# Kernel tuning notes

Hardware: AMD Instinct MI355X
Metric: run time of the kernel (lower is better)

The kernel has to match this reference:

```python
import jax, jax.numpy as jnp
import numpy as np

B, N, DIM, H, DH = 8, 1024, 1024, 16, 64

def setup_inputs() -> dict:
    key = jax.random.key(0)
    ks = jax.random.split(key, 6)
    return {
        'x': jax.random.normal(ks[0], (B, N, DIM), dtype=jnp.float32),
        'freqs': jax.random.normal(ks[1], (1, N, DH), dtype=jnp.float32),
        'bias': jax.random.normal(ks[2], (1, N, DH), dtype=jnp.float32),
        'ln_gamma': jnp.ones((DIM,), jnp.float32),
        'ln_beta': jnp.zeros((DIM,), jnp.float32),
        'w_qk': jax.random.normal(ks[3], (DIM, 2 * H * DH), dtype=jnp.float32) * (DIM ** -0.5),
        'w_v': jax.random.normal(ks[4], (DIM, H * DH), dtype=jnp.float32) * (DIM ** -0.5),
        'w_out': jax.random.normal(ks[5], (H * DH, DIM), dtype=jnp.float32) * ((H * DH) ** -0.5),
        'b_out': jnp.zeros((DIM,), jnp.float32),
    }

def _apply_polar(t, freqs):
    # t: [b,h,n,d]; freqs: [1,n,d] broadcast over b,h. Output doubles last dim.
    t = jax.nn.softplus(t)
    return jnp.concatenate((t * jnp.cos(freqs), t * jnp.sin(freqs)), axis=-1)

def reference(x, freqs, bias, ln_gamma, ln_beta, w_qk, w_v, w_out, b_out):
    eps = 1e-5
    mu = jnp.mean(x, axis=-1, keepdims=True)
    var = jnp.var(x, axis=-1, keepdims=True)
    xn = (x - mu) * jax.lax.rsqrt(var + eps) * ln_gamma + ln_beta
    qk = jnp.einsum('bnd,de->bne', xn, w_qk)
    q, k = jnp.split(qk, 2, axis=-1)
    v = jnp.einsum('bnd,de->bne', xn, w_v)
    split_heads = lambda t: t.reshape(B, N, H, DH).transpose(0, 2, 1, 3)
    q, k, v = split_heads(q), split_heads(k), split_heads(v)
    q = _apply_polar(q, freqs)          # [b,h,n,2*DH]
    k = _apply_polar(k, freqs + bias)   # [b,h,n,2*DH]
    scale = DH ** -0.5
    dots = jnp.einsum('bhnd,bhmd->bhnm', q, k) * scale
    attn = jax.nn.softmax(dots, axis=-1)
    out = jnp.einsum('bhnm,bhmd->bhnd', attn, v)
    out = out.transpose(0, 2, 1, 3).reshape(B, N, H * DH)
    return jnp.einsum('bne,ed->bnd', out, w_out) + b_out
```

## Files before the change

### kernel.cpp

```cpp
#include <hip/hip_runtime.h>
#include <cmath>

using f16   = _Float16;
using f16x2 = __attribute__((ext_vector_type(2))) _Float16;
using f16x4 = __attribute__((ext_vector_type(4))) _Float16;
using f16x8 = __attribute__((ext_vector_type(8))) _Float16;
using f32x4 = __attribute__((ext_vector_type(4))) float;

#define DEV __device__ __forceinline__

constexpr int Bb  = 8;
constexpr int Nn  = 1024;
constexpr int DIM = 1024;
constexpr int Hh  = 16;
constexpr int DH  = 64;
constexpr int EQKV = 3072;

DEV void async16(const f16* g, f16* l) {
  __builtin_amdgcn_global_load_lds(
      (const __attribute__((address_space(1))) void*)g,
      (__attribute__((address_space(3))) void*)l, 16, 0, 0);
}

DEV float softplusf(float x) {
  return fmaxf(x, 0.f) + __logf(1.f + __expf(-fabsf(x)));
}

__global__ __launch_bounds__(256) void transpose_cvt(const float* __restrict__ src,
                                                     f16* __restrict__ dst,
                                                     int rows, int cols) {
  __shared__ float tile[32][33];
  int t = threadIdx.x, tx = t & 31, ty = t >> 5;
  int c0 = blockIdx.x * 32, r0 = blockIdx.y * 32;
#pragma unroll
  for (int j = 0; j < 32; j += 8)
    tile[ty + j][tx] = src[(size_t)(r0 + ty + j) * cols + c0 + tx];
  __syncthreads();
#pragma unroll
  for (int j = 0; j < 32; j += 8)
    dst[(size_t)(c0 + ty + j) * rows + r0 + tx] = (f16)tile[tx][ty + j];
}

__global__ __launch_bounds__(256) void ln_kernel(const float* __restrict__ x,
                                                 const float* __restrict__ gamma,
                                                 const float* __restrict__ beta,
                                                 f16* __restrict__ xn) {
  int row = blockIdx.x;
  int t = threadIdx.x;
  const float4* xr = (const float4*)(x + (size_t)row * DIM);
  float4 v = xr[t];
  float s  = v.x + v.y + v.z + v.w;
  float s2 = v.x * v.x + v.y * v.y + v.z * v.z + v.w * v.w;
#pragma unroll
  for (int off = 32; off; off >>= 1) {
    s  += __shfl_xor(s,  off, 64);
    s2 += __shfl_xor(s2, off, 64);
  }
  __shared__ float red[8];
  int wv = t >> 6, lane = t & 63;
  if (lane == 0) { red[wv] = s; red[4 + wv] = s2; }
  __syncthreads();
  s  = red[0] + red[1] + red[2] + red[3];
  s2 = red[4] + red[5] + red[6] + red[7];
  float mu  = s * (1.f / DIM);
  float var = s2 * (1.f / DIM) - mu * mu;
  float rs  = rsqrtf(var + 1e-5f);
  float4 g = ((const float4*)gamma)[t];
  float4 bb = ((const float4*)beta)[t];
  f16x4 o;
  o[0] = (f16)((v.x - mu) * rs * g.x + bb.x);
  o[1] = (f16)((v.y - mu) * rs * g.y + bb.y);
  o[2] = (f16)((v.z - mu) * rs * g.z + bb.z);
  o[3] = (f16)((v.w - mu) * rs * g.w + bb.w);
  ((f16x4*)(xn + (size_t)row * DIM))[t] = o;
}

template <bool FP32OUT>
__global__ __launch_bounds__(256) void gemm_bt(const f16* __restrict__ A,
                                               const f16* __restrict__ Bt,
                                               void* __restrict__ Cv,
                                               const float* __restrict__ bias,
                                               int M, int K, int E) {
  __shared__ f16 lA[128 * 32];
  __shared__ f16 lB[128 * 32];
  int tid  = threadIdx.x;
  int lane = tid & 63;
  int wv   = __builtin_amdgcn_readfirstlane(tid >> 6);
  int nbe  = E >> 7;
  int bm = blockIdx.x / nbe, be = blockIdx.x % nbe;
  size_t m0 = (size_t)bm * 128, e0 = (size_t)be * 128;
  int wm = (wv & 1) * 64, we = (wv >> 1) * 64;
  int lm = lane & 15, q = lane >> 4;

  f32x4 acc[4][4] = {};

  int row_s[2], cg_s[2];
#pragma unroll
  for (int r = 0; r < 2; ++r) {
    int s = r * 256 + tid;
    row_s[r] = s >> 2;
    cg_s[r]  = (s & 3) ^ ((row_s[r] >> 1) & 3);
  }
  const f16* pa[4];
  const f16* pb[4];
#pragma unroll
  for (int i = 0; i < 4; ++i) {
    int ra = wm + i * 16 + lm;
    pa[i] = lA + ra * 32 + (q ^ ((ra >> 1) & 3)) * 8;
    int rb = we + i * 16 + lm;
    pb[i] = lB + rb * 32 + (q ^ ((rb >> 1) & 3)) * 8;
  }

  for (int k0 = 0; k0 < K; k0 += 32) {
#pragma unroll
    for (int r = 0; r < 2; ++r) {
      const f16* ga = A  + (m0 + row_s[r]) * K + k0 + cg_s[r] * 8;
      const f16* gb = Bt + (e0 + row_s[r]) * K + k0 + cg_s[r] * 8;
      async16(ga, lA + (r * 256 + wv * 64) * 8);
      async16(gb, lB + (r * 256 + wv * 64) * 8);
    }
    __syncthreads();
    f16x8 af[4], bf[4];
#pragma unroll
    for (int i = 0; i < 4; ++i) {
      af[i] = *(const f16x8*)pa[i];
      bf[i] = *(const f16x8*)pb[i];
    }
#pragma unroll
    for (int i = 0; i < 4; ++i)
#pragma unroll
      for (int j = 0; j < 4; ++j)
        acc[i][j] = __builtin_amdgcn_mfma_f32_16x16x32_f16(af[i], bf[j], acc[i][j], 0, 0, 0);
    __syncthreads();
  }

#pragma unroll
  for (int i = 0; i < 4; ++i) {
    size_t mbase = m0 + wm + i * 16 + q * 4;
#pragma unroll
    for (int j = 0; j < 4; ++j) {
      size_t e = e0 + we + j * 16 + lm;
#pragma unroll
      for (int g = 0; g < 4; ++g) {
        float val = acc[i][j][g];
        if (FP32OUT)
          ((float*)Cv)[(mbase + g) * (size_t)E + e] = val + bias[e];
        else
          ((f16*)Cv)[(mbase + g) * (size_t)E + e] = (f16)val;
      }
    }
  }
}

__global__ __launch_bounds__(256) void polar_kernel(const f16* __restrict__ qkv,
                                                    const float* __restrict__ freqs,
                                                    const float* __restrict__ fbias,
                                                    f16* __restrict__ Qp,
                                                    f16* __restrict__ Kp,
                                                    f16* __restrict__ Vt) {
  __shared__ f16 vt[64 * 66];
  int tid = threadIdx.x;
  int bx = blockIdx.x;
  int nt = bx & 15, bh = bx >> 4;
  int b = bh >> 4, h = bh & 15;
  size_t tok0 = (size_t)b * Nn + nt * 64;
  int n0 = nt * 64;
  constexpr float kScale = 0.125f;
#pragma unroll
  for (int i = 0; i < 8; ++i) {
    int e2 = tid + i * 256;
    int nl = e2 >> 5, dp = (e2 & 31) * 2;
    size_t src = (tok0 + nl) * EQKV + h * 64 + dp;
    f16x2 q2 = *(const f16x2*)(qkv + src);
    f16x2 k2 = *(const f16x2*)(qkv + src + 1024);
    f16x2 v2 = *(const f16x2*)(qkv + src + 2048);
    int fidx = (n0 + nl) * 64 + dp;
    float2 f2  = *(const float2*)(freqs + fidx);
    float2 fb2 = *(const float2*)(fbias + fidx);
    f16x2 qc, qs, kc, ksn;
#pragma unroll
    for (int u = 0; u < 2; ++u) {
      float fq = u ? f2.y : f2.x;
      float fk = fq + (u ? fb2.y : fb2.x);
      float spq = softplusf((float)q2[u]) * kScale;
      float spk = softplusf((float)k2[u]);
      float snq, csq, snk, csk;
      __sincosf(fq, &snq, &csq);
      __sincosf(fk, &snk, &csk);
      qc[u]  = (f16)(spq * csq);
      qs[u]  = (f16)(spq * snq);
      kc[u]  = (f16)(spk * csk);
      ksn[u] = (f16)(spk * snk);
    }
    size_t dst = ((size_t)bh * Nn + n0 + nl) * 128 + dp;
    *(f16x2*)(Qp + dst)      = qc;
    *(f16x2*)(Qp + dst + 64) = qs;
    *(f16x2*)(Kp + dst)      = kc;
    *(f16x2*)(Kp + dst + 64) = ksn;
    vt[dp * 66 + nl]       = v2[0];
    vt[(dp + 1) * 66 + nl] = v2[1];
  }
  __syncthreads();
#pragma unroll
  for (int i = 0; i < 16; ++i) {
    int e = tid + i * 256;
    int d = e >> 6, nl = e & 63;
    Vt[((size_t)bh * 64 + d) * Nn + n0 + nl] = vt[d * 66 + nl];
  }
}

constexpr int AK0 = 0;
constexpr int AK1 = 8192;
constexpr int AV0 = 16384;
constexpr int AV1 = 20480;

__global__ __launch_bounds__(512, 6) void attn_kernel(const f16* __restrict__ Qp,
                                                      const f16* __restrict__ Kp,
                                                      const f16* __restrict__ Vt,
                                                      f16* __restrict__ attout) {
  __shared__ f16 smem[24576];

  int tid = threadIdx.x, lane = tid & 63;
  int wv = __builtin_amdgcn_readfirstlane(tid >> 6);
  int lm = lane & 15, q = lane >> 4;
  int bx = blockIdx.x;
  int bh = (bx & 7) | ((bx >> 6) << 3);
  int qt = (bx >> 3) & 7;
  const f16* Kbase = Kp + (size_t)bh * Nn * 128;
  const f16* Vbase = Vt + (size_t)bh * 64 * Nn;

#pragma unroll
  for (int i = 0; i < 2; ++i) {
    int s = i * 512 + tid;
    int r = s >> 4, c = s & 15;
    int g = c ^ (r & 15);
    async16(Kbase + (size_t)r * 128 + g * 8, smem + AK0 + (i * 512 + wv * 64) * 8);
  }
  {
    int r = tid >> 3, c = tid & 7;
    int g = c ^ (r & 7);
    async16(Vbase + (size_t)r * Nn + g * 8, smem + AV0 + (wv * 64) * 8);
  }

  f16x8 qf[4];
  {
    const f16* Qb = Qp + ((size_t)bh * Nn + qt * 128 + wv * 16 + lm) * 128;
#pragma unroll
    for (int ks = 0; ks < 4; ++ks)
      qf[ks] = *(const f16x8*)(Qb + ks * 32 + q * 8);
  }

  f32x4 O[4] = {};
  float mrow = -INFINITY, lrow = 0.f;

  for (int kt = 0; kt < 16; ++kt) {
    __syncthreads();

    if (kt < 15) {
      f16* nK = smem + ((kt & 1) ? AK0 : AK1);
      f16* nV = smem + ((kt & 1) ? AV0 : AV1);
#pragma unroll
      for (int i = 0; i < 2; ++i) {
        int s = i * 512 + tid;
        int r = s >> 4, c = s & 15;
        int g = c ^ (r & 15);
        async16(Kbase + (size_t)((kt + 1) * 64 + r) * 128 + g * 8, nK + (i * 512 + wv * 64) * 8);
      }
      {
        int r = tid >> 3, c = tid & 7;
        int g = c ^ (r & 7);
        async16(Vbase + (size_t)r * Nn + (kt + 1) * 64 + g * 8, nV + (wv * 64) * 8);
      }
    }
    const f16* sK = smem + ((kt & 1) ? AK1 : AK0);
    const f16* sV = smem + ((kt & 1) ? AV1 : AV0);

    f32x4 S[4] = {};
#pragma unroll
    for (int nt = 0; nt < 4; ++nt) {
      f16x8 kf[4];
#pragma unroll
      for (int ks = 0; ks < 4; ++ks)
        kf[ks] = *(const f16x8*)(sK + (nt * 16 + lm) * 128 + (((ks * 4 + q) ^ lm) * 8));
#pragma unroll
      for (int ks = 0; ks < 4; ++ks)
        S[nt] = __builtin_amdgcn_mfma_f32_16x16x32_f16(kf[ks], qf[ks], S[nt], 0, 0, 0);
    }

    float mx = -INFINITY;
#pragma unroll
    for (int nt = 0; nt < 4; ++nt)
#pragma unroll
      for (int g = 0; g < 4; ++g) mx = fmaxf(mx, S[nt][g]);
    mx = fmaxf(mx, __shfl_xor(mx, 16, 64));
    mx = fmaxf(mx, __shfl_xor(mx, 32, 64));
    float mn = fmaxf(mrow, mx);
    float alpha = __expf(mrow - mn);
    mrow = mn;
    float rs = 0.f;
    f16x4 pf[4];
#pragma unroll
    for (int nt = 0; nt < 4; ++nt) {
#pragma unroll
      for (int g = 0; g < 4; ++g) {
        float p = __expf(S[nt][g] - mn);
        S[nt][g] = p;
        rs += p;
      }
      pf[nt][0] = (f16)S[nt][0];
      pf[nt][1] = (f16)S[nt][1];
      pf[nt][2] = (f16)S[nt][2];
      pf[nt][3] = (f16)S[nt][3];
    }
    rs += __shfl_xor(rs, 16, 64);
    rs += __shfl_xor(rs, 32, 64);
    lrow = lrow * alpha + rs;
#pragma unroll
    for (int nto = 0; nto < 4; ++nto)
#pragma unroll
      for (int g = 0; g < 4; ++g) O[nto][g] *= alpha;

#pragma unroll
    for (int nto = 0; nto < 4; ++nto) {
      int r = nto * 16 + lm;
#pragma unroll
      for (int nt = 0; nt < 4; ++nt) {
        int c16 = (nt * 2 + (q >> 1)) ^ (r & 7);
        f16x4 vf = *(const f16x4*)(sV + r * 64 + c16 * 8 + (q & 1) * 4);
        O[nto] = __builtin_amdgcn_mfma_f32_16x16x16f16(vf, pf[nt], O[nto], 0, 0, 0);
      }
    }
  }

  int b = bh >> 4, h = bh & 15;
  size_t token = (size_t)b * Nn + qt * 128 + wv * 16 + lm;
  float inv = 1.f / lrow;
#pragma unroll
  for (int nto = 0; nto < 4; ++nto) {
    f16x4 o4;
#pragma unroll
    for (int g = 0; g < 4; ++g) o4[g] = (f16)(O[nto][g] * inv);
    *(f16x4*)(attout + token * (size_t)(Hh * DH) + h * 64 + nto * 16 + q * 4) = o4;
  }
}

extern "C" void kernel_launch(void* const* d_in, const int* in_sizes, int n_in,
                              void* d_out, int out_size, void* d_ws, size_t ws_size,
                              hipStream_t stream) {
  const float* x     = (const float*)d_in[0];
  const float* freqs = (const float*)d_in[1];
  const float* fbias = (const float*)d_in[2];
  const float* gamma = (const float*)d_in[3];
  const float* beta  = (const float*)d_in[4];
  const float* w_qk  = (const float*)d_in[5];
  const float* w_v   = (const float*)d_in[6];
  const float* w_out = (const float*)d_in[7];
  const float* b_out = (const float*)d_in[8];
  float* out = (float*)d_out;

  const size_t T = (size_t)Bb * Nn;
  f16* WqkvT = (f16*)d_ws;
  f16* WoutT = WqkvT + (size_t)EQKV * DIM;
  f16* Xn    = WoutT + (size_t)DIM * DIM;
  f16* QKV   = Xn + T * DIM;
  f16* AttO  = QKV + T * EQKV;
  f16* Qp    = AttO + T * DIM;
  f16* Kp    = Qp + (size_t)128 * Nn * 128;
  f16* Vt    = Kp + (size_t)128 * Nn * 128;

  transpose_cvt<<<dim3(2048 / 32, 1024 / 32), 256, 0, stream>>>(w_qk, WqkvT, DIM, 2048);
  transpose_cvt<<<dim3(1024 / 32, 1024 / 32), 256, 0, stream>>>(w_v, WqkvT + (size_t)2048 * DIM, DIM, 1024);
  transpose_cvt<<<dim3(1024 / 32, 1024 / 32), 256, 0, stream>>>(w_out, WoutT, DIM, DIM);

  ln_kernel<<<(int)T, 256, 0, stream>>>(x, gamma, beta, Xn);

  gemm_bt<false><<<(int)(T / 128) * (EQKV / 128), 256, 0, stream>>>(
      Xn, WqkvT, (void*)QKV, nullptr, (int)T, DIM, EQKV);

  polar_kernel<<<Bb * Hh * (Nn / 64), 256, 0, stream>>>(QKV, freqs, fbias, Qp, Kp, Vt);

  attn_kernel<<<Bb * Hh * (Nn / 128), 512, 0, stream>>>(Qp, Kp, Vt, AttO);

  gemm_bt<true><<<(int)(T / 128) * (DIM / 128), 256, 0, stream>>>(
      AttO, WoutT, (void*)out, b_out, (int)T, DIM, DIM);
}
```

Baseline: 315.9 us.

## Process two query groups per wave in attention and fold row-sum into MFMA

The attention kernel moves from 8 waves of 16 query rows to 4 waves of 32 rows each, so every K fragment read from LDS feeds two MFMAs. The softmax row sum is now computed by the PV MFMA itself: an extra row of ones is appended to the V tile, replacing the per-tile shuffle reductions. The three weight transpose launches are merged into one grid. In exchange, register pressure per wave rises, fewer waves are resident for latency hiding, and the extra ones row adds MFMA work.

Result: no change. 311.9 us (-1.3%).

```diff
diff --git a/kernel.cpp b/kernel.cpp
--- a/kernel.cpp
+++ b/kernel.cpp
@@ -26,19 +26,27 @@
   return fmaxf(x, 0.f) + __logf(1.f + __expf(-fabsf(x)));
 }
 
-__global__ __launch_bounds__(256) void transpose_cvt(const float* __restrict__ src,
-                                                     f16* __restrict__ dst,
-                                                     int rows, int cols) {
+__global__ __launch_bounds__(256) void transpose_cvt3(const float* __restrict__ s0,
+                                                      const float* __restrict__ s1,
+                                                      const float* __restrict__ s2,
+                                                      f16* __restrict__ d0,
+                                                      f16* __restrict__ d2) {
   __shared__ float tile[32][33];
+  const float* src; f16* dst; int cols;
+  int bz = blockIdx.z;
+  if (bz == 0)      { src = s0; dst = d0;                        cols = 2048; }
+  else if (bz == 1) { src = s1; dst = d0 + (size_t)2048 * 1024;  cols = 1024; }
+  else              { src = s2; dst = d2;                        cols = 1024; }
+  int c0 = blockIdx.x * 32, r0 = blockIdx.y * 32;
+  if (c0 >= cols) return;
   int t = threadIdx.x, tx = t & 31, ty = t >> 5;
-  int c0 = blockIdx.x * 32, r0 = blockIdx.y * 32;
 #pragma unroll
   for (int j = 0; j < 32; j += 8)
     tile[ty + j][tx] = src[(size_t)(r0 + ty + j) * cols + c0 + tx];
   __syncthreads();
 #pragma unroll
   for (int j = 0; j < 32; j += 8)
-    dst[(size_t)(c0 + ty + j) * rows + r0 + tx] = (f16)tile[tx][ty + j];
+    dst[(size_t)(c0 + ty + j) * 1024 + r0 + tx] = (f16)tile[tx][ty + j];
 }
 
 __global__ __launch_bounds__(256) void ln_kernel(const float* __restrict__ x,
@@ -209,16 +217,17 @@
   }
 }
 
-constexpr int AK0 = 0;
-constexpr int AK1 = 8192;
-constexpr int AV0 = 16384;
-constexpr int AV1 = 20480;
-
-__global__ __launch_bounds__(512, 6) void attn_kernel(const f16* __restrict__ Qp,
+constexpr int VK0 = 0;
+constexpr int VK1 = 8192;
+constexpr int VV0 = 16384;
+constexpr int VV1 = 21504;
+constexpr int VEND = 26624;
+
+__global__ __launch_bounds__(256, 3) void attn_kernel(const f16* __restrict__ Qp,
                                                       const f16* __restrict__ Kp,
                                                       const f16* __restrict__ Vt,
                                                       f16* __restrict__ attout) {
-  __shared__ f16 smem[24576];
+  __shared__ f16 smem[VEND];
 
   int tid = threadIdx.x, lane = tid & 63;
   int wv = __builtin_amdgcn_readfirstlane(tid >> 6);
@@ -229,53 +238,67 @@
   const f16* Kbase = Kp + (size_t)bh * Nn * 128;
   const f16* Vbase = Vt + (size_t)bh * 64 * Nn;
 
-#pragma unroll
-  for (int i = 0; i < 2; ++i) {
-    int s = i * 512 + tid;
+  {
+    int idx = tid * 4;
+    f16 val = (idx < 64) ? (f16)1.0f : (f16)0.0f;
+    f16x4 v4 = {val, val, val, val};
+    *(f16x4*)(smem + VV0 + 64 * 64 + idx) = v4;
+    *(f16x4*)(smem + VV1 + 64 * 64 + idx) = v4;
+  }
+
+#pragma unroll
+  for (int i = 0; i < 4; ++i) {
+    int s = i * 256 + tid;
     int r = s >> 4, c = s & 15;
     int g = c ^ (r & 15);
-    async16(Kbase + (size_t)r * 128 + g * 8, smem + AK0 + (i * 512 + wv * 64) * 8);
-  }
+    async16(Kbase + (size_t)r * 128 + g * 8, smem + VK0 + (i * 256 + wv * 64) * 8);
+  }
+#pragma unroll
+  for (int i = 0; i < 2; ++i) {
+    int s = i * 256 + tid;
+    int r = s >> 3, c = s & 7;
+    int g = c ^ (r & 7);
+    async16(Vbase + (size_t)r * Nn + g * 8, smem + VV0 + (i * 256 + wv * 64) * 8);
+  }
+
+  f16x8 qf[2][4];
   {
-    int r = tid >> 3, c = tid & 7;
-    int g = c ^ (r & 7);
-    async16(Vbase + (size_t)r * Nn + g * 8, smem + AV0 + (wv * 64) * 8);
-  }
-
-  f16x8 qf[4];
-  {
-    const f16* Qb = Qp + ((size_t)bh * Nn + qt * 128 + wv * 16 + lm) * 128;
-#pragma unroll
-    for (int ks = 0; ks < 4; ++ks)
-      qf[ks] = *(const f16x8*)(Qb + ks * 32 + q * 8);
-  }
-
-  f32x4 O[4] = {};
-  float mrow = -INFINITY, lrow = 0.f;
+    const f16* Qb = Qp + ((size_t)bh * Nn + qt * 128 + wv * 32) * 128;
+#pragma unroll
+    for (int grp = 0; grp < 2; ++grp)
+#pragma unroll
+      for (int ks = 0; ks < 4; ++ks)
+        qf[grp][ks] = *(const f16x8*)(Qb + (size_t)(grp * 16 + lm) * 128 + ks * 32 + q * 8);
+  }
+
+  f32x4 O[2][5] = {};
+  float mrow[2] = {-INFINITY, -INFINITY};
 
   for (int kt = 0; kt < 16; ++kt) {
     __syncthreads();
 
     if (kt < 15) {
-      f16* nK = smem + ((kt & 1) ? AK0 : AK1);
-      f16* nV = smem + ((kt & 1) ? AV0 : AV1);
-#pragma unroll
-      for (int i = 0; i < 2; ++i) {
-        int s = i * 512 + tid;
+      f16* nK = smem + ((kt & 1) ? VK0 : VK1);
+      f16* nV = smem + ((kt & 1) ? VV0 : VV1);
+#pragma unroll
+      for (int i = 0; i < 4; ++i) {
+        int s = i * 256 + tid;
         int r = s >> 4, c = s & 15;
         int g = c ^ (r & 15);
-        async16(Kbase + (size_t)((kt + 1) * 64 + r) * 128 + g * 8, nK + (i * 512 + wv * 64) * 8);
+        async16(Kbase + (size_t)((kt + 1) * 64 + r) * 128 + g * 8, nK + (i * 256 + wv * 64) * 8);
       }
-      {
-        int r = tid >> 3, c = tid & 7;
+#pragma unroll
+      for (int i = 0; i < 2; ++i) {
+        int s = i * 256 + tid;
+        int r = s >> 3, c = s & 7;
         int g = c ^ (r & 7);
-        async16(Vbase + (size_t)r * Nn + (kt + 1) * 64 + g * 8, nV + (wv * 64) * 8);
+        async16(Vbase + (size_t)r * Nn + (kt + 1) * 64 + g * 8, nV + (i * 256 + wv * 64) * 8);
       }
     }
-    const f16* sK = smem + ((kt & 1) ? AK1 : AK0);
-    const f16* sV = smem + ((kt & 1) ? AV1 : AV0);
-
-    f32x4 S[4] = {};
+    const f16* sK = smem + ((kt & 1) ? VK1 : VK0);
+    const f16* sV = smem + ((kt & 1) ? VV1 : VV0);
+
+    f32x4 S[2][4] = {};
 #pragma unroll
     for (int nt = 0; nt < 4; ++nt) {
       f16x8 kf[4];
@@ -283,64 +306,62 @@
       for (int ks = 0; ks < 4; ++ks)
         kf[ks] = *(const f16x8*)(sK + (nt * 16 + lm) * 128 + (((ks * 4 + q) ^ lm) * 8));
 #pragma unroll
-      for (int ks = 0; ks < 4; ++ks)
-        S[nt] = __builtin_amdgcn_mfma_f32_16x16x32_f16(kf[ks], qf[ks], S[nt], 0, 0, 0);
-    }
-
-    float mx = -INFINITY;
-#pragma unroll
-    for (int nt = 0; nt < 4; ++nt)
-#pragma unroll
-      for (int g = 0; g < 4; ++g) mx = fmaxf(mx, S[nt][g]);
-    mx = fmaxf(mx, __shfl_xor(mx, 16, 64));
-    mx = fmaxf(mx, __shfl_xor(mx, 32, 64));
-    float mn = fmaxf(mrow, mx);
-    float alpha = __expf(mrow - mn);
-    mrow = mn;
-    float rs = 0.f;
-    f16x4 pf[4];
-#pragma unroll
-    for (int nt = 0; nt < 4; ++nt) {
-#pragma unroll
-      for (int g = 0; g < 4; ++g) {
-        float p = __expf(S[nt][g] - mn);
-        S[nt][g] = p;
-        rs += p;
+      for (int ks = 0; ks < 4; ++ks) {
+        S[0][nt] = __builtin_amdgcn_mfma_f32_16x16x32_f16(kf[ks], qf[0][ks], S[0][nt], 0, 0, 0);
+        S[1][nt] = __builtin_amdgcn_mfma_f32_16x16x32_f16(kf[ks], qf[1][ks], S[1][nt], 0, 0, 0);
       }
-      pf[nt][0] = (f16)S[nt][0];
-      pf[nt][1] = (f16)S[nt][1];
-      pf[nt][2] = (f16)S[nt][2];
-      pf[nt][3] = (f16)S[nt][3];
-    }
-    rs += __shfl_xor(rs, 16, 64);
-    rs += __shfl_xor(rs, 32, 64);
-    lrow = lrow * alpha + rs;
-#pragma unroll
-    for (int nto = 0; nto < 4; ++nto)
-#pragma unroll
-      for (int g = 0; g < 4; ++g) O[nto][g] *= alpha;
-
-#pragma unroll
-    for (int nto = 0; nto < 4; ++nto) {
+    }
+
+    f16x4 pf[2][4];
+#pragma unroll
+    for (int grp = 0; grp < 2; ++grp) {
+      float mx = -INFINITY;
+#pragma unroll
+      for (int nt = 0; nt < 4; ++nt)
+#pragma unroll
+        for (int g = 0; g < 4; ++g) mx = fmaxf(mx, S[grp][nt][g]);
+      mx = fmaxf(mx, __shfl_xor(mx, 16, 64));
+      mx = fmaxf(mx, __shfl_xor(mx, 32, 64));
+      float mn = fmaxf(mrow[grp], mx);
+      float alpha = __expf(mrow[grp] - mn);
+      mrow[grp] = mn;
+#pragma unroll
+      for (int nt = 0; nt < 4; ++nt)
+#pragma unroll
+        for (int g = 0; g < 4; ++g)
+          pf[grp][nt][g] = (f16)__expf(S[grp][nt][g] - mn);
+#pragma unroll
+      for (int nto = 0; nto < 5; ++nto)
+#pragma unroll
+        for (int g = 0; g < 4; ++g) O[grp][nto][g] *= alpha;
+    }
+
+#pragma unroll
+    for (int nto = 0; nto < 5; ++nto) {
       int r = nto * 16 + lm;
 #pragma unroll
       for (int nt = 0; nt < 4; ++nt) {
         int c16 = (nt * 2 + (q >> 1)) ^ (r & 7);
         f16x4 vf = *(const f16x4*)(sV + r * 64 + c16 * 8 + (q & 1) * 4);
-        O[nto] = __builtin_amdgcn_mfma_f32_16x16x16f16(vf, pf[nt], O[nto], 0, 0, 0);
+        O[0][nto] = __builtin_amdgcn_mfma_f32_16x16x16f16(vf, pf[0][nt], O[0][nto], 0, 0, 0);
+        O[1][nto] = __builtin_amdgcn_mfma_f32_16x16x16f16(vf, pf[1][nt], O[1][nto], 0, 0, 0);
       }
     }
   }
 
   int b = bh >> 4, h = bh & 15;
-  size_t token = (size_t)b * Nn + qt * 128 + wv * 16 + lm;
-  float inv = 1.f / lrow;
-#pragma unroll
-  for (int nto = 0; nto < 4; ++nto) {
-    f16x4 o4;
-#pragma unroll
-    for (int g = 0; g < 4; ++g) o4[g] = (f16)(O[nto][g] * inv);
-    *(f16x4*)(attout + token * (size_t)(Hh * DH) + h * 64 + nto * 16 + q * 4) = o4;
+#pragma unroll
+  for (int grp = 0; grp < 2; ++grp) {
+    float l = __shfl(O[grp][4][0], lm, 64);
+    float inv = 1.f / l;
+    size_t token = (size_t)b * Nn + qt * 128 + wv * 32 + grp * 16 + lm;
+#pragma unroll
+    for (int nto = 0; nto < 4; ++nto) {
+      f16x4 o4;
+#pragma unroll
+      for (int g = 0; g < 4; ++g) o4[g] = (f16)(O[grp][nto][g] * inv);
+      *(f16x4*)(attout + token * (size_t)(Hh * DH) + h * 64 + nto * 16 + q * 4) = o4;
+    }
   }
 }
 
@@ -368,9 +389,7 @@
   f16* Kp    = Qp + (size_t)128 * Nn * 128;
   f16* Vt    = Kp + (size_t)128 * Nn * 128;
 
-  transpose_cvt<<<dim3(2048 / 32, 1024 / 32), 256, 0, stream>>>(w_qk, WqkvT, DIM, 2048);
-  transpose_cvt<<<dim3(1024 / 32, 1024 / 32), 256, 0, stream>>>(w_v, WqkvT + (size_t)2048 * DIM, DIM, 1024);
-  transpose_cvt<<<dim3(1024 / 32, 1024 / 32), 256, 0, stream>>>(w_out, WoutT, DIM, DIM);
+  transpose_cvt3<<<dim3(64, 32, 3), 256, 0, stream>>>(w_qk, w_v, w_out, WqkvT, WoutT);
 
   ln_kernel<<<(int)T, 256, 0, stream>>>(x, gamma, beta, Xn);
 
@@ -379,7 +398,7 @@
 
   polar_kernel<<<Bb * Hh * (Nn / 64), 256, 0, stream>>>(QKV, freqs, fbias, Qp, Kp, Vt);
 
-  attn_kernel<<<Bb * Hh * (Nn / 128), 512, 0, stream>>>(Qp, Kp, Vt, AttO);
+  attn_kernel<<<Bb * Hh * (Nn / 128), 256, 0, stream>>>(Qp, Kp, Vt, AttO);
 
   gemm_bt<true><<<(int)(T / 128) * (DIM / 128), 256, 0, stream>>>(
       AttO, WoutT, (void*)out, b_out, (int)T, DIM, DIM);
```
